# Performance work log

Measured on AMD Instinct MI355X. Metric: run time of the kernel, lower is better.

## Reference

```python
import jax, jax.numpy as jnp
import numpy as np
from math import sqrt

B, S, D_MODEL = 2, 2048, 1024
H = 16
ADIM = D_MODEL // H  # 64
K_REL = 16
N_PEMB = 2 * K_REL + 1  # 33, bidirectional rel-pos vocabulary


def setup_inputs() -> dict:
    key = jax.random.key(0)
    ks = jax.random.split(key, 8)
    sc = 0.02
    return {
        "iQ": jax.random.normal(ks[0], (B, S, D_MODEL), jnp.float32),
        "iK": jax.random.normal(ks[1], (B, S, D_MODEL), jnp.float32),
        "iV": jax.random.normal(ks[2], (B, S, D_MODEL), jnp.float32),
        "Wq": jax.random.normal(ks[3], (D_MODEL, D_MODEL), jnp.float32) * sc,
        "Wk": jax.random.normal(ks[4], (D_MODEL, D_MODEL), jnp.float32) * sc,
        "Wv": jax.random.normal(ks[5], (D_MODEL, D_MODEL), jnp.float32) * sc,
        "Wo": jax.random.normal(ks[6], (D_MODEL, D_MODEL), jnp.float32) * sc,
        "rel_pemb": jax.random.normal(ks[7], (N_PEMB, ADIM), jnp.float32) * sc,
    }


def reference(iQ, iK, iV, Wq, Wk, Wv, Wo, rel_pemb):
    b, nq, _ = iQ.shape
    seql = iK.shape[1]
    # projections -> [b, h, len, d]
    q = (iQ @ Wq).reshape(b, nq, H, ADIM).transpose(0, 2, 1, 3)
    k = (iK @ Wk).reshape(b, seql, H, ADIM).transpose(0, 2, 1, 3)
    v = (iV @ Wv).reshape(b, seql, H, ADIM).transpose(0, 2, 1, 3)
    # content scores: [b, h, nq, seql]
    scores = jnp.einsum("bhqd,bhsd->bhqs", q, k)
    # relative position bias: rel[i, j] = clamp(j - i, -K, K) + K
    pos = jnp.arange(seql)
    rel = jnp.clip(pos[None, :] - pos[:, None], -K_REL, K_REL) + K_REL
    rel = rel[seql - nq:, :]  # narrow to query rows: [nq, seql]
    e = rel_pemb[rel]  # [nq, seql, d]
    scores = scores + jnp.einsum("bhqd,qsd->bhqs", q, e)
    scores = scores / sqrt(ADIM)
    attn = jax.nn.softmax(scores, axis=-1)
    ctx = jnp.einsum("bhqs,bhsd->bqhd", attn, v).reshape(b, nq, H * ADIM)
    return ctx @ Wo
```

## Files before the change

kernel.cpp:

```cpp
#include <hip/hip_runtime.h>
#include <hip/hip_bf16.h>

#define BB 2
#define S 2048
#define DM 1024
#define H 16
#define ADIM 64
#define NP 33

typedef __bf16 bf16x8 __attribute__((ext_vector_type(8)));
typedef float f32x4 __attribute__((ext_vector_type(4)));

__device__ __forceinline__ void gload16(const void* g, void* l) {
  __builtin_amdgcn_global_load_lds(
      (__attribute__((address_space(1))) void*)(g),
      (__attribute__((address_space(3))) void*)(l), 16, 0, 0);
}

__global__ __launch_bounds__(256) void tobf16(
    const float* __restrict__ X0, const float* __restrict__ X1,
    const float* __restrict__ X2, __bf16* __restrict__ Y0,
    __bf16* __restrict__ Y1, __bf16* __restrict__ Y2) {
  const float* X; __bf16* Y;
  switch (blockIdx.z) {
    case 0: X = X0; Y = Y0; break;
    case 1: X = X1; Y = Y1; break;
    default: X = X2; Y = Y2; break;
  }
  size_t i = ((size_t)blockIdx.x * 256 + threadIdx.x) * 8;
  float4 a0 = *(const float4*)(X + i);
  float4 a1 = *(const float4*)(X + i + 4);
  bf16x8 v;
  v[0] = (__bf16)a0.x; v[1] = (__bf16)a0.y;
  v[2] = (__bf16)a0.z; v[3] = (__bf16)a0.w;
  v[4] = (__bf16)a1.x; v[5] = (__bf16)a1.y;
  v[6] = (__bf16)a1.z; v[7] = (__bf16)a1.w;
  *(bf16x8*)(Y + i) = v;
}

__global__ __launch_bounds__(256) void wtrans(
    const float* __restrict__ W0, const float* __restrict__ W1,
    const float* __restrict__ W2, __bf16* __restrict__ T0,
    __bf16* __restrict__ T1, __bf16* __restrict__ T2) {
  const float* W; __bf16* T;
  switch (blockIdx.z) {
    case 0: W = W0; T = T0; break;
    case 1: W = W1; T = T1; break;
    default: W = W2; T = T2; break;
  }
  __shared__ __bf16 tile[64][65];
  int j = threadIdx.x & 63, i0 = threadIdx.x >> 6;
  int n0 = blockIdx.x * 64, k0 = blockIdx.y * 64;
#pragma unroll
  for (int p = 0; p < 16; ++p) {
    int i = i0 + p * 4;
    tile[i][j] = (__bf16)W[(size_t)(k0 + i) * DM + n0 + j];
  }
  __syncthreads();
#pragma unroll
  for (int p = 0; p < 16; ++p) {
    int i = i0 + p * 4;
    T[(size_t)(n0 + i) * DM + k0 + j] = tile[j][i];
  }
}

#define LDK 40
template <bool A_FP32, int BN, typename CT>
__device__ __forceinline__ void gemm_body(const void* __restrict__ Av,
                                          const __bf16* __restrict__ BT,
                                          CT* __restrict__ C, int mode,
                                          int m0, int n0) {
  constexpr int NF = BN / 32;
  constexpr int BH = BN / 16;
  __shared__ __align__(16) __bf16 As[128 * LDK];
  __shared__ __align__(16) __bf16 Bs[BN * 32];
  int t = threadIdx.x;
  int w = t >> 6, lane = t & 63, l15 = lane & 15, quad = lane >> 4;
  int wm = w >> 1, wn = w & 1;
  constexpr int LA = A_FP32 ? LDK : 32;
  f32x4 acc[4][NF] = {};
  int lr = t >> 2;
  int lk = (t & 3) * 8;
  int r4 = lane >> 2;
  int c8 = (lane & 3) * 8;
  for (int k0 = 0; k0 < DM; k0 += 32) {
    if constexpr (A_FP32) {
#pragma unroll
      for (int rr = 0; rr < 2; ++rr) {
        int row = rr * 64 + lr;
        const float* src = (const float*)Av + (size_t)(m0 + row) * DM + k0 + lk;
        float4 a0 = *(const float4*)src;
        float4 a1 = *(const float4*)(src + 4);
        bf16x8 v;
        v[0] = (__bf16)a0.x; v[1] = (__bf16)a0.y;
        v[2] = (__bf16)a0.z; v[3] = (__bf16)a0.w;
        v[4] = (__bf16)a1.x; v[5] = (__bf16)a1.y;
        v[6] = (__bf16)a1.z; v[7] = (__bf16)a1.w;
        *(bf16x8*)&As[row * LDK + lk] = v;
      }
    } else {
#pragma unroll
      for (int q = 0; q < 2; ++q) {
        int half = w * 2 + q;
        gload16((const __bf16*)Av + (size_t)(m0 + half * 16 + r4) * DM + k0 + c8,
                &As[half * 512]);
      }
    }
#pragma unroll
    for (int q = 0; q < BH / 4; ++q) {
      int half = w * (BH / 4) + q;
      gload16(&BT[(size_t)(n0 + half * 16 + r4) * DM + k0 + c8],
              &Bs[half * 512]);
    }
    __syncthreads();
    bf16x8 af[4], bfr[NF];
#pragma unroll
    for (int mi = 0; mi < 4; ++mi)
      af[mi] = *(const bf16x8*)&As[(wm * 64 + mi * 16 + l15) * LA + quad * 8];
#pragma unroll
    for (int ni = 0; ni < NF; ++ni)
      bfr[ni] =
          *(const bf16x8*)&Bs[(wn * (BN / 2) + ni * 16 + l15) * 32 + quad * 8];
#pragma unroll
    for (int mi = 0; mi < 4; ++mi)
#pragma unroll
      for (int ni = 0; ni < NF; ++ni)
        acc[mi][ni] = __builtin_amdgcn_mfma_f32_16x16x32_bf16(
            af[mi], bfr[ni], acc[mi][ni], 0, 0, 0);
    __syncthreads();
  }
#pragma unroll
  for (int mi = 0; mi < 4; ++mi)
#pragma unroll
    for (int ni = 0; ni < NF; ++ni)
#pragma unroll
      for (int r = 0; r < 4; ++r) {
        int row = m0 + wm * 64 + mi * 16 + quad * 4 + r;
        int col = n0 + wn * (BN / 2) + ni * 16 + l15;
        CT v = (CT)acc[mi][ni][r];
        if (mode == 0) {
          C[(size_t)row * DM + col] = v;
        } else {
          int b = row >> 11, s = row & (S - 1);
          int h = col >> 6, d = col & (ADIM - 1);
          if (mode == 1)
            C[((size_t)(b * H + h) * S + s) * ADIM + d] = v;
          else
            C[((size_t)(b * H + h) * ADIM + d) * S + s] = v;
        }
      }
}

__global__ __launch_bounds__(256) void proj3(
    const float* __restrict__ iQ, const float* __restrict__ iK,
    const float* __restrict__ iV, const __bf16* __restrict__ WqT,
    const __bf16* __restrict__ WkT, const __bf16* __restrict__ WvT,
    __bf16* __restrict__ Qw, __bf16* __restrict__ Kw,
    __bf16* __restrict__ Vt) {
  const float* A; const __bf16* B; __bf16* C; int mode;
  switch (blockIdx.z) {
    case 0: A = iQ; B = WqT; C = Qw; mode = 1; break;
    case 1: A = iK; B = WkT; C = Kw; mode = 1; break;
    default: A = iV; B = WvT; C = Vt; mode = 2; break;
  }
  int i2 = blockIdx.x + (blockIdx.y << 3);
  int xcd = i2 & 7, slot = i2 >> 3;
  int m0 = (xcd + ((slot >> 3) << 3)) * 128;
  int n0 = (slot & 7) * 128;
  gemm_body<true, 128, __bf16>(A, B, C, mode, m0, n0);
}

__global__ __launch_bounds__(256) void proj3b(
    const __bf16* __restrict__ Qb, const __bf16* __restrict__ Kb,
    const __bf16* __restrict__ Vb, const __bf16* __restrict__ WqT,
    const __bf16* __restrict__ WkT, const __bf16* __restrict__ WvT,
    __bf16* __restrict__ Qw, __bf16* __restrict__ Kw,
    __bf16* __restrict__ Vt) {
  const __bf16* A; const __bf16* B; __bf16* C; int mode;
  switch (blockIdx.z) {
    case 0: A = Qb; B = WqT; C = Qw; mode = 1; break;
    case 1: A = Kb; B = WkT; C = Kw; mode = 1; break;
    default: A = Vb; B = WvT; C = Vt; mode = 2; break;
  }
  int i2 = blockIdx.x + (blockIdx.y << 3);
  int xcd = i2 & 7, slot = i2 >> 3;
  int m0 = (xcd + ((slot >> 3) << 3)) * 128;
  int n0 = (slot & 7) * 128;
  gemm_body<false, 128, __bf16>(A, B, C, mode, m0, n0);
}

__global__ __launch_bounds__(256) void gemm_final(
    const __bf16* __restrict__ ctx, const __bf16* __restrict__ WoT,
    float* __restrict__ out) {
  int i2 = blockIdx.x + (blockIdx.y << 4);
  int xcd = i2 & 7, slot = i2 >> 3;
  int m0 = ((xcd << 2) + (slot >> 4)) * 128;
  int n0 = (slot & 15) * 64;
  gemm_body<false, 64, float>(ctx, WoT, out, 0, m0, n0);
}

#define AST 72
__global__ __launch_bounds__(256) void attn_flash(
    const __bf16* __restrict__ Qw, const __bf16* __restrict__ Kw,
    const __bf16* __restrict__ Vt, const float* __restrict__ pemb,
    __bf16* __restrict__ ctx) {
  int i = blockIdx.x + (blockIdx.y << 5);
  int a = i & 7, m = i >> 3;
  int bh = m >> 2;
  int q0 = ((a << 2) + (m & 3)) * 64;
  int b = bh >> 4, h = bh & 15;
  int t = threadIdx.x, w = t >> 6, lane = t & 63, l15 = lane & 15,
      quad = lane >> 4;
  const __bf16* Qh = Qw + (size_t)bh * S * ADIM;
  const __bf16* Kh = Kw + (size_t)bh * S * ADIM;
  const __bf16* Vh = Vt + (size_t)bh * ADIM * S;

  __shared__ __align__(16) char smem[36352];
  __bf16* Ks = (__bf16*)smem;
  __bf16* Vs = (__bf16*)(smem + 9216);
  float* pband = (float*)(smem + 18432);
  __bf16* pbufw = (__bf16*)(smem + 27136 + w * 2304);
  __bf16* peb = (__bf16*)smem;

  for (int ii = t; ii < 48 * 64; ii += 256) {
    int r = ii >> 6, d = ii & 63;
    peb[r * AST + d] = (r < NP) ? (__bf16)pemb[ii] : (__bf16)0.f;
  }

  int qa = q0 + w * 16 + l15;
  bf16x8 qf0 = *(const bf16x8*)&Qh[(size_t)qa * ADIM + quad * 8];
  bf16x8 qf1 = *(const bf16x8*)&Qh[(size_t)qa * ADIM + 32 + quad * 8];
  __syncthreads();

  {
    f32x4 pc[3] = {};
#pragma unroll
    for (int ni = 0; ni < 3; ++ni) {
      bf16x8 b0 = *(const bf16x8*)&peb[(ni * 16 + l15) * AST + quad * 8];
      bf16x8 b1 = *(const bf16x8*)&peb[(ni * 16 + l15) * AST + 32 + quad * 8];
      pc[ni] = __builtin_amdgcn_mfma_f32_16x16x32_bf16(qf0, b0, pc[ni], 0, 0, 0);
      pc[ni] = __builtin_amdgcn_mfma_f32_16x16x32_bf16(qf1, b1, pc[ni], 0, 0, 0);
    }
#pragma unroll
    for (int ni = 0; ni < 3; ++ni)
#pragma unroll
      for (int r = 0; r < 4; ++r) {
        int col = ni * 16 + l15;
        if (col < NP) pband[(w * 16 + quad * 4 + r) * 34 + col] = pc[ni][r];
      }
  }
  __syncthreads();

  int qc = q0 + w * 16 + quad * 4;
  int lrow = w * 16 + quad * 4;
  int qw0 = q0 + w * 16;
  float lsum[4] = {0.f, 0.f, 0.f, 0.f};
  f32x4 o[4] = {};

  const float K2 = 0.18033688011112f;
  float pK0[4], pK32[4];
#pragma unroll
  for (int r = 0; r < 4; ++r) {
    pK0[r] = pband[(lrow + r) * 34 + 0] * K2;
    pK32[r] = pband[(lrow + r) * 34 + 32] * K2;
  }

  int srow = t >> 3;
  int scol = (t & 7) * 8;
  bf16x8 k0r = *(const bf16x8*)&Kh[(size_t)srow * ADIM + scol];
  bf16x8 k1r = *(const bf16x8*)&Kh[(size_t)(32 + srow) * ADIM + scol];
  bf16x8 v0r = *(const bf16x8*)&Vh[(size_t)srow * S + scol];
  bf16x8 v1r = *(const bf16x8*)&Vh[(size_t)(32 + srow) * S + scol];

  for (int s0 = 0; s0 < S; s0 += 64) {
    __syncthreads();
    *(bf16x8*)&Ks[srow * AST + scol] = k0r;
    *(bf16x8*)&Ks[(32 + srow) * AST + scol] = k1r;
    *(bf16x8*)&Vs[srow * AST + scol] = v0r;
    *(bf16x8*)&Vs[(32 + srow) * AST + scol] = v1r;
    int sn = s0 + 64;
    if (sn < S) {
      k0r = *(const bf16x8*)&Kh[(size_t)(sn + srow) * ADIM + scol];
      k1r = *(const bf16x8*)&Kh[(size_t)(sn + 32 + srow) * ADIM + scol];
      v0r = *(const bf16x8*)&Vh[(size_t)srow * S + sn + scol];
      v1r = *(const bf16x8*)&Vh[(size_t)(32 + srow) * S + sn + scol];
    }
    __syncthreads();

    f32x4 c[4];
#pragma unroll
    for (int j = 0; j < 4; ++j) {
      f32x4 cj = {};
      bf16x8 kb0 = *(const bf16x8*)&Ks[(j * 16 + l15) * AST + quad * 8];
      bf16x8 kb1 = *(const bf16x8*)&Ks[(j * 16 + l15) * AST + 32 + quad * 8];
      cj = __builtin_amdgcn_mfma_f32_16x16x32_bf16(qf0, kb0, cj, 0, 0, 0);
      cj = __builtin_amdgcn_mfma_f32_16x16x32_bf16(qf1, kb1, cj, 0, 0, 0);
      c[j] = cj;
    }

    float pv[4][4];
    bool below = (s0 + 79 <= qw0);
    bool above = (s0 >= qw0 + 31);
    if (below || above) {
#pragma unroll
      for (int j = 0; j < 4; ++j)
#pragma unroll
        for (int r = 0; r < 4; ++r) {
          float pk = below ? pK0[r] : pK32[r];
          float e = exp2f(__builtin_fmaf(c[j][r], K2, pk));
          lsum[r] += e;
          pv[j][r] = e;
        }
    } else {
#pragma unroll
      for (int j = 0; j < 4; ++j)
#pragma unroll
        for (int r = 0; r < 4; ++r) {
          int qg = qc + r;
          int sg = s0 + j * 16 + l15;
          int i0 = sg - qg; i0 = i0 < -16 ? -16 : (i0 > 16 ? 16 : i0); i0 += 16;
          float e = exp2f((c[j][r] + pband[(lrow + r) * 34 + i0]) * K2);
          lsum[r] += e;
          pv[j][r] = e;
        }
    }

#pragma unroll
    for (int j = 0; j < 4; ++j)
#pragma unroll
      for (int r = 0; r < 4; ++r)
        pbufw[(quad * 4 + r) * AST + j * 16 + l15] = (__bf16)pv[j][r];
    bf16x8 pa0 = *(const bf16x8*)&pbufw[l15 * AST + quad * 8];
    bf16x8 pa1 = *(const bf16x8*)&pbufw[l15 * AST + 32 + quad * 8];

#pragma unroll
    for (int nt = 0; nt < 4; ++nt) {
      bf16x8 vb0 = *(const bf16x8*)&Vs[(nt * 16 + l15) * AST + quad * 8];
      bf16x8 vb1 = *(const bf16x8*)&Vs[(nt * 16 + l15) * AST + 32 + quad * 8];
      o[nt] = __builtin_amdgcn_mfma_f32_16x16x32_bf16(pa0, vb0, o[nt], 0, 0, 0);
      o[nt] = __builtin_amdgcn_mfma_f32_16x16x32_bf16(pa1, vb1, o[nt], 0, 0, 0);
    }
  }

#pragma unroll
  for (int r = 0; r < 4; ++r) {
#pragma unroll
    for (int mm = 1; mm < 16; mm <<= 1) lsum[r] += __shfl_xor(lsum[r], mm, 64);
  }
#pragma unroll
  for (int nt = 0; nt < 4; ++nt)
#pragma unroll
    for (int r = 0; r < 4; ++r) {
      int qg = qc + r;
      int d = nt * 16 + l15;
      ctx[(size_t)(b * S + qg) * DM + h * ADIM + d] =
          (__bf16)(o[nt][r] / lsum[r]);
    }
}

extern "C" void kernel_launch(void* const* d_in, const int* in_sizes, int n_in,
                              void* d_out, int out_size, void* d_ws,
                              size_t ws_size, hipStream_t stream) {
  bool sizes_ok =
      (n_in == 8 && in_sizes[0] == BB * S * DM && in_sizes[1] == BB * S * DM &&
       in_sizes[2] == BB * S * DM && in_sizes[3] == DM * DM &&
       in_sizes[4] == DM * DM && in_sizes[5] == DM * DM &&
       in_sizes[6] == DM * DM && in_sizes[7] == NP * ADIM &&
       out_size == BB * S * DM);
  if (!sizes_ok) return;
  if (ws_size < 33ull * 1024 * 1024) return;

  const float* iQ = (const float*)d_in[0];
  const float* iK = (const float*)d_in[1];
  const float* iV = (const float*)d_in[2];
  const float* Wq = (const float*)d_in[3];
  const float* Wk = (const float*)d_in[4];
  const float* Wv = (const float*)d_in[5];
  const float* Wo = (const float*)d_in[6];
  const float* pemb = (const float*)d_in[7];

  char* w = (char*)d_ws;
  const size_t MB = 1024 * 1024;
  __bf16* Qw  = (__bf16*)(w + 0 * MB);
  __bf16* Kw  = (__bf16*)(w + 8 * MB);
  __bf16* Vt  = (__bf16*)(w + 16 * MB);
  __bf16* ctx = (__bf16*)(w + 24 * MB);
  __bf16* WqT = (__bf16*)(w + 24 * MB);
  __bf16* WkT = (__bf16*)(w + 26 * MB);
  __bf16* WvT = (__bf16*)(w + 28 * MB);
  __bf16* WoT = (__bf16*)(w + 0 * MB);

  wtrans<<<dim3(16, 16, 3), 256, 0, stream>>>(Wq, Wk, Wv, WqT, WkT, WvT);
  if (ws_size >= 56ull * 1024 * 1024) {
    __bf16* Qb = (__bf16*)(w + 32 * MB);
    __bf16* Kb = (__bf16*)(w + 40 * MB);
    __bf16* Vb = (__bf16*)(w + 48 * MB);
    tobf16<<<dim3(2048, 1, 3), 256, 0, stream>>>(iQ, iK, iV, Qb, Kb, Vb);
    proj3b<<<dim3(8, 32, 3), 256, 0, stream>>>(Qb, Kb, Vb, WqT, WkT, WvT,
                                               Qw, Kw, Vt);
  } else {
    proj3<<<dim3(8, 32, 3), 256, 0, stream>>>(iQ, iK, iV, WqT, WkT, WvT,
                                              Qw, Kw, Vt);
  }
  attn_flash<<<dim3(S / 64, BB * H), 256, 0, stream>>>(Qw, Kw, Vt, pemb, ctx);
  wtrans<<<dim3(16, 16, 1), 256, 0, stream>>>(Wo, Wo, Wo, WoT, WoT, WoT);
  gemm_final<<<dim3(16, 32), 256, 0, stream>>>(ctx, WoT, (float*)d_out);
}
```

Measured before the change: 257.4 us.

## Compute V projection transposed for coalesced Vt stores and regroup attention blocks per XCD

The V projection is split into its own kernel that computes WvT·Vbᵀ, so the transposed Vt output is written contiguously along the sequence dimension instead of with strided scatter stores. Q and K projections move into a two-slice launch. Attention blocks are remapped so each XCD handles whole heads, which should improve L2 reuse of K and V tiles. The softmax switches from exp2f with a prescaled log2e constant to __expf with a 1/8 scale. The cost is one extra kernel launch and an unswizzled grid for the V GEMM.

```diff
diff --git a/kernel.cpp b/kernel.cpp
--- a/kernel.cpp
+++ b/kernel.cpp
@@ -140,6 +140,10 @@
         CT v = (CT)acc[mi][ni][r];
         if (mode == 0) {
           C[(size_t)row * DM + col] = v;
+        } else if (mode == 3) {
+          int hh = row >> 6, dd = row & (ADIM - 1);
+          int bb = col >> 11, ss = col & (S - 1);
+          C[((size_t)(bb * H + hh) * ADIM + dd) * S + ss] = v;
         } else {
           int b = row >> 11, s = row & (S - 1);
           int h = col >> 6, d = col & (ADIM - 1);
@@ -170,23 +174,26 @@
   gemm_body<true, 128, __bf16>(A, B, C, mode, m0, n0);
 }
 
-__global__ __launch_bounds__(256) void proj3b(
+__global__ __launch_bounds__(256) void proj2b(
     const __bf16* __restrict__ Qb, const __bf16* __restrict__ Kb,
-    const __bf16* __restrict__ Vb, const __bf16* __restrict__ WqT,
-    const __bf16* __restrict__ WkT, const __bf16* __restrict__ WvT,
-    __bf16* __restrict__ Qw, __bf16* __restrict__ Kw,
-    __bf16* __restrict__ Vt) {
-  const __bf16* A; const __bf16* B; __bf16* C; int mode;
-  switch (blockIdx.z) {
-    case 0: A = Qb; B = WqT; C = Qw; mode = 1; break;
-    case 1: A = Kb; B = WkT; C = Kw; mode = 1; break;
-    default: A = Vb; B = WvT; C = Vt; mode = 2; break;
-  }
+    const __bf16* __restrict__ WqT, const __bf16* __restrict__ WkT,
+    __bf16* __restrict__ Qw, __bf16* __restrict__ Kw) {
+  const __bf16* A; const __bf16* B; __bf16* C;
+  if (blockIdx.z == 0) { A = Qb; B = WqT; C = Qw; }
+  else                 { A = Kb; B = WkT; C = Kw; }
   int i2 = blockIdx.x + (blockIdx.y << 3);
   int xcd = i2 & 7, slot = i2 >> 3;
   int m0 = (xcd + ((slot >> 3) << 3)) * 128;
   int n0 = (slot & 7) * 128;
-  gemm_body<false, 128, __bf16>(A, B, C, mode, m0, n0);
+  gemm_body<false, 128, __bf16>(A, B, C, 1, m0, n0);
+}
+
+__global__ __launch_bounds__(256) void projV(
+    const __bf16* __restrict__ WvT, const __bf16* __restrict__ Vb,
+    __bf16* __restrict__ Vt) {
+  int m0 = blockIdx.y * 128;
+  int n0 = blockIdx.x * 128;
+  gemm_body<false, 128, __bf16>(WvT, Vb, Vt, 3, m0, n0);
 }
 
 __global__ __launch_bounds__(256) void gemm_final(
@@ -205,9 +212,9 @@
     const __bf16* __restrict__ Vt, const float* __restrict__ pemb,
     __bf16* __restrict__ ctx) {
   int i = blockIdx.x + (blockIdx.y << 5);
-  int a = i & 7, m = i >> 3;
-  int bh = m >> 2;
-  int q0 = ((a << 2) + (m & 3)) * 64;
+  int a = i & 7, j = i >> 3;
+  int bh = (a << 2) + (j >> 5);
+  int q0 = (j & 31) * 64;
   int b = bh >> 4, h = bh & 15;
   int t = threadIdx.x, w = t >> 6, lane = t & 63, l15 = lane & 15,
       quad = lane >> 4;
@@ -257,12 +264,11 @@
   float lsum[4] = {0.f, 0.f, 0.f, 0.f};
   f32x4 o[4] = {};
 
-  const float K2 = 0.18033688011112f;
-  float pK0[4], pK32[4];
+  float pb0[4], pb32[4];
 #pragma unroll
   for (int r = 0; r < 4; ++r) {
-    pK0[r] = pband[(lrow + r) * 34 + 0] * K2;
-    pK32[r] = pband[(lrow + r) * 34 + 32] * K2;
+    pb0[r] = pband[(lrow + r) * 34 + 0] * 0.125f;
+    pb32[r] = pband[(lrow + r) * 34 + 32] * 0.125f;
   }
 
   int srow = t >> 3;
@@ -289,13 +295,13 @@
 
     f32x4 c[4];
 #pragma unroll
-    for (int j = 0; j < 4; ++j) {
+    for (int jj = 0; jj < 4; ++jj) {
       f32x4 cj = {};
-      bf16x8 kb0 = *(const bf16x8*)&Ks[(j * 16 + l15) * AST + quad * 8];
-      bf16x8 kb1 = *(const bf16x8*)&Ks[(j * 16 + l15) * AST + 32 + quad * 8];
+      bf16x8 kb0 = *(const bf16x8*)&Ks[(jj * 16 + l15) * AST + quad * 8];
+      bf16x8 kb1 = *(const bf16x8*)&Ks[(jj * 16 + l15) * AST + 32 + quad * 8];
       cj = __builtin_amdgcn_mfma_f32_16x16x32_bf16(qf0, kb0, cj, 0, 0, 0);
       cj = __builtin_amdgcn_mfma_f32_16x16x32_bf16(qf1, kb1, cj, 0, 0, 0);
-      c[j] = cj;
+      c[jj] = cj;
     }
 
     float pv[4][4];
@@ -303,33 +309,33 @@
     bool above = (s0 >= qw0 + 31);
     if (below || above) {
 #pragma unroll
-      for (int j = 0; j < 4; ++j)
+      for (int jj = 0; jj < 4; ++jj)
 #pragma unroll
         for (int r = 0; r < 4; ++r) {
-          float pk = below ? pK0[r] : pK32[r];
-          float e = exp2f(__builtin_fmaf(c[j][r], K2, pk));
+          float pb = below ? pb0[r] : pb32[r];
+          float e = __expf(__builtin_fmaf(c[jj][r], 0.125f, pb));
           lsum[r] += e;
-          pv[j][r] = e;
+          pv[jj][r] = e;
         }
     } else {
 #pragma unroll
-      for (int j = 0; j < 4; ++j)
+      for (int jj = 0; jj < 4; ++jj)
 #pragma unroll
         for (int r = 0; r < 4; ++r) {
           int qg = qc + r;
-          int sg = s0 + j * 16 + l15;
+          int sg = s0 + jj * 16 + l15;
           int i0 = sg - qg; i0 = i0 < -16 ? -16 : (i0 > 16 ? 16 : i0); i0 += 16;
-          float e = exp2f((c[j][r] + pband[(lrow + r) * 34 + i0]) * K2);
+          float e = __expf((c[jj][r] + pband[(lrow + r) * 34 + i0]) * 0.125f);
           lsum[r] += e;
-          pv[j][r] = e;
+          pv[jj][r] = e;
         }
     }
 
 #pragma unroll
-    for (int j = 0; j < 4; ++j)
+    for (int jj = 0; jj < 4; ++jj)
 #pragma unroll
       for (int r = 0; r < 4; ++r)
-        pbufw[(quad * 4 + r) * AST + j * 16 + l15] = (__bf16)pv[j][r];
+        pbufw[(quad * 4 + r) * AST + jj * 16 + l15] = (__bf16)pv[jj][r];
     bf16x8 pa0 = *(const bf16x8*)&pbufw[l15 * AST + quad * 8];
     bf16x8 pa1 = *(const bf16x8*)&pbufw[l15 * AST + 32 + quad * 8];
 
@@ -396,8 +402,8 @@
     __bf16* Kb = (__bf16*)(w + 40 * MB);
     __bf16* Vb = (__bf16*)(w + 48 * MB);
     tobf16<<<dim3(2048, 1, 3), 256, 0, stream>>>(iQ, iK, iV, Qb, Kb, Vb);
-    proj3b<<<dim3(8, 32, 3), 256, 0, stream>>>(Qb, Kb, Vb, WqT, WkT, WvT,
-                                               Qw, Kw, Vt);
+    proj2b<<<dim3(8, 32, 2), 256, 0, stream>>>(Qb, Kb, WqT, WkT, Qw, Kw);
+    projV<<<dim3(32, 8), 256, 0, stream>>>(WvT, Vb, Vt);
   } else {
     proj3<<<dim3(8, 32, 3), 256, 0, stream>>>(iQ, iK, iV, WqT, WkT, WvT,
                                               Qw, Kw, Vt);
```

Result: no change. 259.8 us (+0.9%).
